# Optimization experiments

Hardware: AMD Instinct MI355X
Metric: run time of the kernel (lower is better)

The kernel has to match this reference:

```python
import jax, jax.numpy as jnp
import numpy as np

WIN = 5  # mask_window_size


def gather_windows(indices, image, win):
    """Gather win x win windows of pixel features centered at each query index.
    indices: [Q, 2] (y, x) int; image: [H, W, F].
    Returns keys [Q, win, win, F] (zeros at out-of-bounds) and pad mask [Q, win, win]."""
    H, W = image.shape[0], image.shape[1]
    offs = jnp.arange(win) - win // 2
    yy = (indices[:, 0, None] + offs)[:, :, None]
    xx = (indices[:, 1, None] + offs)[:, None, :]
    pad = (yy < 0) | (yy >= H) | (xx < 0) | (xx >= W)
    yc = jnp.clip(yy, 0, H - 1)
    xc = jnp.clip(xx, 0, W - 1)
    keys = image[yc, xc]
    keys = jnp.where(pad[..., None], jnp.zeros((), keys.dtype), keys)
    return keys, pad


def mlp(x, w1, b1, w2, b2):
    return jax.nn.relu(x @ w1 + b1) @ w2 + b2


def setup_inputs() -> dict:
    key = jax.random.key(0)
    ks = jax.random.split(key, 8)
    Q, Dq, F, Hd = 16384, 128, 128, 256
    H, W = 1024, 1024
    return {
        "queries": jax.random.normal(ks[0], (Q, Dq), jnp.float32),
        "query_indices": jax.random.randint(ks[1], (Q, 2), 0, H),
        "image": jax.random.normal(ks[2], (H, W, F), jnp.float32),
        "pm_w1": jax.random.normal(ks[3], (F, Hd), jnp.float32) * 0.02,
        "pm_b1": jnp.zeros((Hd,), jnp.float32),
        "pm_w2": jax.random.normal(ks[4], (Hd, Dq), jnp.float32) * 0.02,
        "pm_b2": jnp.zeros((Dq,), jnp.float32),
        "qp_w1": jax.random.normal(ks[5], (Dq, Hd), jnp.float32) * 0.02,
        "qp_b1": jnp.zeros((Hd,), jnp.float32),
        "qp_w2": jax.random.normal(ks[6], (Hd, F), jnp.float32) * 0.02,
        "qp_b2": jnp.zeros((F,), jnp.float32),
    }


def reference(queries, query_indices, image, pm_w1, pm_b1, pm_w2, pm_b2,
              qp_w1, qp_b1, qp_w2, qp_b2):
    # windowed key gather with out-of-bounds padding
    mask_keys, key_pad_mask = gather_windows(query_indices, image, WIN)  # [Q,w,w,F]
    # pixel_mask_head on gathered keys: F -> hidden -> query_dim
    mlped_mask_keys = mlp(mask_keys, pm_w1, pm_b1, pm_w2, pm_b2)          # [Q,w,w,Dq]
    binary_mask_logits = jnp.einsum('qf,qhwf->qhw', queries, mlped_mask_keys)
    # query_portion_head on queries: query_dim -> hidden -> F
    mlped_queries = mlp(queries, qp_w1, qp_b1, qp_w2, qp_b2)              # [Q,F]
    portion_logits = jnp.einsum('qf,qhwf->qhw', mlped_queries, mask_keys)
    # additive -inf pad bias (matches masked_fill + add in torch)
    pad_bias = jnp.where(key_pad_mask, -jnp.inf, 0.0).astype(binary_mask_logits.dtype)
    binary_mask_logits = binary_mask_logits + pad_bias
    portion_logits = portion_logits + pad_bias
    nonzero_key_mask = jnp.any(mask_keys != 0, axis=-1)
    return binary_mask_logits, portion_logits, nonzero_key_mask
```

## Files before the change

### kernel.cpp

```cpp
#include <hip/hip_runtime.h>
#include <math.h>

#define NEG_SENTINEL (-3.0e38f)


typedef __bf16 bf16_t;
typedef __bf16 bf16x8 __attribute__((ext_vector_type(8)));
typedef float  f32x4  __attribute__((ext_vector_type(4)));

#define MFMA(a, b, c) __builtin_amdgcn_mfma_f32_16x16x32_bf16((a), (b), (c), 0, 0, 0)

__device__ inline bf16x8 cvt_bf16x8(float4 a, float4 b) {
  bf16x8 r;
  r[0] = (bf16_t)a.x; r[1] = (bf16_t)a.y; r[2] = (bf16_t)a.z; r[3] = (bf16_t)a.w;
  r[4] = (bf16_t)b.x; r[5] = (bf16_t)b.y; r[6] = (bf16_t)b.z; r[7] = (bf16_t)b.w;
  return r;
}

__global__ __launch_bounds__(256) void prep_kernel(
    const float* __restrict__ pm_w1, const float* __restrict__ qp_w1,
    const float* __restrict__ qp_w2, const float* __restrict__ pm_w2,
    bf16_t* __restrict__ w1t, bf16_t* __restrict__ qw1t,
    bf16_t* __restrict__ qw2t, bf16_t* __restrict__ w2pm)
{
  int i = blockIdx.x * 256 + threadIdx.x;
  int m = i >> 15, e = i & 32767;
  if (m == 0)      { int n = e >> 7, k = e & 127; w1t[e]  = (bf16_t)pm_w1[k * 256 + n]; }
  else if (m == 1) { int n = e >> 7, k = e & 127; qw1t[e] = (bf16_t)qp_w1[k * 256 + n]; }
  else if (m == 2) { int f = e >> 8, h = e & 255; qw2t[e] = (bf16_t)qp_w2[h * 128 + f]; }
  else             { w2pm[e] = (bf16_t)pm_w2[e]; }
}

__global__ __launch_bounds__(256) void query_side_kernel(
    const float* __restrict__ queries,
    const float* __restrict__ pm_b2,
    const float* __restrict__ qp_b1, const float* __restrict__ qp_b2,
    const bf16_t* __restrict__ qw1t, const bf16_t* __restrict__ w2pm,
    const bf16_t* __restrict__ qw2t,
    bf16_t* __restrict__ v_ws, bf16_t* __restrict__ mq_ws, float* __restrict__ c_ws)
{
  __shared__ float qb1_lds[256];
  __shared__ float qb2_lds[128];
  __shared__ __align__(16) bf16_t hq_lds[4][4096];

  const int t = threadIdx.x;
  const int w = t >> 6, l = t & 63, lr = l & 15, lg = l >> 4;
  const int qb = blockIdx.x * 64;
  const int qrow = qb + w * 16 + lr;

  for (int i = t; i < 256; i += 256) qb1_lds[i] = qp_b1[i];
  if (t < 128) qb2_lds[t] = qp_b2[t];

  bf16x8 aq[4];
  float cpart = 0.f;
  const float* qp = queries + (size_t)qrow * 128;
  #pragma unroll
  for (int s = 0; s < 4; ++s) {
    int k0 = s * 32 + lg * 8;
    float4 u0 = *(const float4*)(qp + k0);
    float4 u1 = *(const float4*)(qp + k0 + 4);
    float4 b0 = *(const float4*)(pm_b2 + k0);
    float4 b1 = *(const float4*)(pm_b2 + k0 + 4);
    cpart += u0.x*b0.x + u0.y*b0.y + u0.z*b0.z + u0.w*b0.w
           + u1.x*b1.x + u1.y*b1.y + u1.z*b1.z + u1.w*b1.w;
    aq[s] = cvt_bf16x8(u0, u1);
  }
  cpart += __shfl_xor(cpart, 16);
  cpart += __shfl_xor(cpart, 32);
  if (l < 16) c_ws[qb + w * 16 + l] = cpart;

  __syncthreads();

  bf16_t* hqw = hq_lds[w];

  #pragma unroll 2
  for (int n = 0; n < 16; ++n) {
    f32x4 aa = {0.f, 0.f, 0.f, 0.f};
    f32x4 ac = {0.f, 0.f, 0.f, 0.f};
    const int col = n * 16 + lr;
    #pragma unroll
    for (int s = 0; s < 4; ++s) {
      bf16x8 ba = *(const bf16x8*)(qw1t + (size_t)col * 128 + (s * 4 + lg) * 8);
      bf16x8 bc = *(const bf16x8*)(w2pm + (size_t)col * 128 + (s * 4 + lg) * 8);
      aa = MFMA(aq[s], ba, aa);
      ac = MFMA(aq[s], bc, ac);
    }
    float bv = qb1_lds[col];
    const int k8 = col >> 3;
    #pragma unroll
    for (int j = 0; j < 4; ++j) {
      int rw = lg * 4 + j;
      float hv = fmaxf(aa[j] + bv, 0.f);
      hqw[rw * 256 + ((k8 ^ rw) * 8) + (col & 7)] = (bf16_t)hv;
      v_ws[(size_t)(qb + w * 16 + rw) * 256 + col] = (bf16_t)ac[j];
    }
  }

  __syncthreads();

  bf16x8 ah[8];
  #pragma unroll
  for (int s = 0; s < 8; ++s)
    ah[s] = *(const bf16x8*)(hqw + lr * 256 + (((s * 4 + lg) ^ lr) * 8));
  #pragma unroll 2
  for (int n = 0; n < 8; ++n) {
    f32x4 am = {0.f, 0.f, 0.f, 0.f};
    const int col = n * 16 + lr;
    #pragma unroll
    for (int s = 0; s < 8; ++s) {
      bf16x8 bm = *(const bf16x8*)(qw2t + (size_t)col * 256 + (s * 4 + lg) * 8);
      am = MFMA(ah[s], bm, am);
    }
    float bv = qb2_lds[col];
    #pragma unroll
    for (int j = 0; j < 4; ++j)
      mq_ws[(size_t)(qb + w * 16 + lg * 4 + j) * 128 + col] = (bf16_t)(am[j] + bv);
  }
}

__global__ __launch_bounds__(320, 2) void window_kernel(
    const int* __restrict__ qidx, const float* __restrict__ image,
    const float* __restrict__ pm_b1,
    const bf16_t* __restrict__ w1t_g,
    const bf16_t* __restrict__ v_ws, const bf16_t* __restrict__ mq_ws,
    const float* __restrict__ c_ws, float* __restrict__ out, int Q)
{
  __shared__ __align__(16) float v_lds[16 * 256];
  __shared__ __align__(16) float mq_lds[16 * 128];
  __shared__ float b1_lds[256];
  __shared__ float c_lds[16];
  __shared__ unsigned char pad_lds[400];

  const int t = threadIdx.x;
  const int w = t >> 6, l = t & 63, lr = l & 15, lg = l >> 4;
  const int qb = blockIdx.x * 16;

  bf16x8 afr[5][4];
  int aq[5], apad[5], nzf[5];
  #pragma unroll
  for (int tt = 0; tt < 5; ++tt) {
    int r = w * 80 + tt * 16 + lr;
    int ql = r / 25;
    int cell = r - ql * 25;
    int dy = cell / 5 - 2;
    int dx = cell - (dy + 2) * 5 - 2;
    int yy = qidx[2 * (qb + ql) + 0] + dy;
    int xx = qidx[2 * (qb + ql) + 1] + dx;
    bool pad = (yy < 0) | (yy >= 1024) | (xx < 0) | (xx >= 1024);
    aq[tt] = ql; apad[tt] = pad ? 1 : 0;
    if (l < 16) pad_lds[r] = (unsigned char)(pad ? 1 : 0);
    const float* px = image + (size_t)(pad ? 0 : (yy * 1024 + xx)) * 128;
    int nz = 0;
    #pragma unroll
    for (int s = 0; s < 4; ++s) {
      float4 u0 = make_float4(0.f, 0.f, 0.f, 0.f), u1 = u0;
      if (!pad) {
        u0 = *(const float4*)(px + s * 32 + lg * 8);
        u1 = *(const float4*)(px + s * 32 + lg * 8 + 4);
      }
      nz |= (u0.x != 0.f) | (u0.y != 0.f) | (u0.z != 0.f) | (u0.w != 0.f)
          | (u1.x != 0.f) | (u1.y != 0.f) | (u1.z != 0.f) | (u1.w != 0.f);
      afr[tt][s] = cvt_bf16x8(u0, u1);
    }
    nzf[tt] = nz;
  }

  {
    const bf16_t* vg = v_ws + (size_t)qb * 256;
    for (int i = t; i < 512; i += 320) {
      bf16x8 d = *(const bf16x8*)(vg + i * 8);
      float4 lo = make_float4((float)d[0], (float)d[1], (float)d[2], (float)d[3]);
      float4 hi = make_float4((float)d[4], (float)d[5], (float)d[6], (float)d[7]);
      *(float4*)(v_lds + i * 8) = lo;
      *(float4*)(v_lds + i * 8 + 4) = hi;
    }
  }
  {
    const bf16_t* mg = mq_ws + (size_t)qb * 128;
    for (int i = t; i < 256; i += 320) {
      bf16x8 d = *(const bf16x8*)(mg + i * 8);
      float4 lo = make_float4((float)d[0], (float)d[1], (float)d[2], (float)d[3]);
      float4 hi = make_float4((float)d[4], (float)d[5], (float)d[6], (float)d[7]);
      *(float4*)(mq_lds + i * 8) = lo;
      *(float4*)(mq_lds + i * 8 + 4) = hi;
    }
  }
  for (int i = t; i < 256; i += 320) b1_lds[i] = pm_b1[i];
  if (t < 16) c_lds[t] = c_ws[qb + t];

  __syncthreads();

  #pragma unroll
  for (int tt = 0; tt < 5; ++tt) {
    const float* mrow = mq_lds + aq[tt] * 128;
    float pp = 0.f;
    #pragma unroll
    for (int s = 0; s < 4; ++s) {
      const float* m = mrow + s * 32 + lg * 8;
      float4 m0 = *(const float4*)(m);
      float4 m1 = *(const float4*)(m + 4);
      bf16x8 a = afr[tt][s];
      pp += (float)a[0]*m0.x + (float)a[1]*m0.y + (float)a[2]*m0.z + (float)a[3]*m0.w
          + (float)a[4]*m1.x + (float)a[5]*m1.y + (float)a[6]*m1.z + (float)a[7]*m1.w;
    }
    pp += __shfl_xor(pp, 16);
    pp += __shfl_xor(pp, 32);
    int nz = nzf[tt];
    nz |= __shfl_xor(nz, 16);
    nz |= __shfl_xor(nz, 32);
    if (l < 16) {
      int r = w * 80 + tt * 16 + l;
      int ql = aq[tt];
      int cell = r - ql * 25;
      int q = qb + ql;
      out[(size_t)Q * 25 + (size_t)q * 25 + cell]     = apad[tt] ? NEG_SENTINEL : pp;
      out[(size_t)2 * Q * 25 + (size_t)q * 25 + cell] = nz ? 1.0f : 0.0f;
    }
  }

  int vb[5][4];
  #pragma unroll
  for (int tt = 0; tt < 5; ++tt) {
    #pragma unroll
    for (int j = 0; j < 4; ++j) {
      int rc = w * 80 + tt * 16 + lg * 4 + j;
      vb[tt][j] = (rc / 25) * 256 + lr;
    }
  }
  float part[5][4];
  #pragma unroll
  for (int tt = 0; tt < 5; ++tt)
    #pragma unroll
    for (int j = 0; j < 4; ++j) part[tt][j] = 0.f;

  #pragma unroll 2
  for (int n = 0; n < 16; ++n) {
    bf16x8 b[4];
    #pragma unroll
    for (int s = 0; s < 4; ++s)
      b[s] = *(const bf16x8*)(w1t_g + (size_t)(n * 16 + lr) * 128 + (s * 4 + lg) * 8);
    float bv = b1_lds[n * 16 + lr];
    #pragma unroll
    for (int tt = 0; tt < 5; ++tt) {
      f32x4 acc = {0.f, 0.f, 0.f, 0.f};
      #pragma unroll
      for (int s = 0; s < 4; ++s) acc = MFMA(afr[tt][s], b[s], acc);
      #pragma unroll
      for (int j = 0; j < 4; ++j) {
        float hv = fmaxf(acc[j] + bv, 0.f);
        part[tt][j] = fmaf(hv, v_lds[vb[tt][j] + n * 16], part[tt][j]);
      }
    }
  }

  #pragma unroll
  for (int tt = 0; tt < 5; ++tt) {
    #pragma unroll
    for (int j = 0; j < 4; ++j) {
      float s = part[tt][j];
      s += __shfl_xor(s, 1);
      s += __shfl_xor(s, 2);
      s += __shfl_xor(s, 4);
      s += __shfl_xor(s, 8);
      if (lr == 0) {
        int rc = w * 80 + tt * 16 + lg * 4 + j;
        int q = rc / 25, cell = rc - q * 25;
        out[(size_t)(qb + q) * 25 + cell] =
            pad_lds[rc] ? NEG_SENTINEL : (s + c_lds[q]);
      }
    }
  }
}

extern "C" void kernel_launch(void* const* d_in, const int* in_sizes, int n_in,
                              void* d_out, int out_size, void* d_ws, size_t ws_size,
                              hipStream_t stream) {
  const float* queries = (const float*)d_in[0];
  const int*   qidx    = (const int*)d_in[1];
  const float* image   = (const float*)d_in[2];
  const float* pm_w1   = (const float*)d_in[3];
  const float* pm_b1   = (const float*)d_in[4];
  const float* pm_w2   = (const float*)d_in[5];
  const float* pm_b2   = (const float*)d_in[6];
  const float* qp_w1   = (const float*)d_in[7];
  const float* qp_b1   = (const float*)d_in[8];
  const float* qp_w2   = (const float*)d_in[9];
  const float* qp_b2   = (const float*)d_in[10];
  float* out = (float*)d_out;

  const int Q = in_sizes[0] / 128;

  char* ws = (char*)d_ws;
  bf16_t* v_ws  = (bf16_t*)ws;  ws += (size_t)Q * 256 * 2;
  bf16_t* mq_ws = (bf16_t*)ws;  ws += (size_t)Q * 128 * 2;
  float*  c_ws  = (float*)ws;   ws += (size_t)Q * 4;
  bf16_t* w1t   = (bf16_t*)ws;  ws += 32768 * 2;
  bf16_t* qw1t  = (bf16_t*)ws;  ws += 32768 * 2;
  bf16_t* qw2t  = (bf16_t*)ws;  ws += 32768 * 2;
  bf16_t* w2pm  = (bf16_t*)ws;  ws += 32768 * 2;

  prep_kernel<<<512, 256, 0, stream>>>(pm_w1, qp_w1, qp_w2, pm_w2,
                                       w1t, qw1t, qw2t, w2pm);
  query_side_kernel<<<Q / 64, 256, 0, stream>>>(queries, pm_b2, qp_b1, qp_b2,
                                                qw1t, w2pm, qw2t, v_ws, mq_ws, c_ws);
  window_kernel<<<Q / 16, 320, 0, stream>>>(qidx, image, pm_b1, w1t,
                                            v_ws, mq_ws, c_ws, out, Q);
}
```

Measured before the change: 733.6 us.

## Fuse query-side MLP into window kernel, computing per-block query results in LDS

Drops the separate query-side kernel. Each 16-query window block now computes its own query MLP, the W2-projected query vector and the bias dot product with four of its five waves, and keeps the results in LDS instead of a global workspace. This removes a kernel launch and the bf16 round trip of the v/mq/c intermediates through global memory. In exchange it adds LDS usage (an extra hq buffer, bias arrays) and two more block barriers, and the query-side MFMA work now runs at 16 queries per block with the fifth wave idle during it.

New measurement: 729.2 us. About the same (-0.6%).

```diff
diff --git a/kernel.cpp b/kernel.cpp
--- a/kernel.cpp
+++ b/kernel.cpp
@@ -31,102 +31,20 @@
   else             { w2pm[e] = (bf16_t)pm_w2[e]; }
 }
 
-__global__ __launch_bounds__(256) void query_side_kernel(
+__global__ __launch_bounds__(320, 2) void fused_kernel(
     const float* __restrict__ queries,
-    const float* __restrict__ pm_b2,
+    const int* __restrict__ qidx, const float* __restrict__ image,
+    const float* __restrict__ pm_b1, const float* __restrict__ pm_b2,
     const float* __restrict__ qp_b1, const float* __restrict__ qp_b2,
-    const bf16_t* __restrict__ qw1t, const bf16_t* __restrict__ w2pm,
-    const bf16_t* __restrict__ qw2t,
-    bf16_t* __restrict__ v_ws, bf16_t* __restrict__ mq_ws, float* __restrict__ c_ws)
-{
-  __shared__ float qb1_lds[256];
-  __shared__ float qb2_lds[128];
-  __shared__ __align__(16) bf16_t hq_lds[4][4096];
-
-  const int t = threadIdx.x;
-  const int w = t >> 6, l = t & 63, lr = l & 15, lg = l >> 4;
-  const int qb = blockIdx.x * 64;
-  const int qrow = qb + w * 16 + lr;
-
-  for (int i = t; i < 256; i += 256) qb1_lds[i] = qp_b1[i];
-  if (t < 128) qb2_lds[t] = qp_b2[t];
-
-  bf16x8 aq[4];
-  float cpart = 0.f;
-  const float* qp = queries + (size_t)qrow * 128;
-  #pragma unroll
-  for (int s = 0; s < 4; ++s) {
-    int k0 = s * 32 + lg * 8;
-    float4 u0 = *(const float4*)(qp + k0);
-    float4 u1 = *(const float4*)(qp + k0 + 4);
-    float4 b0 = *(const float4*)(pm_b2 + k0);
-    float4 b1 = *(const float4*)(pm_b2 + k0 + 4);
-    cpart += u0.x*b0.x + u0.y*b0.y + u0.z*b0.z + u0.w*b0.w
-           + u1.x*b1.x + u1.y*b1.y + u1.z*b1.z + u1.w*b1.w;
-    aq[s] = cvt_bf16x8(u0, u1);
-  }
-  cpart += __shfl_xor(cpart, 16);
-  cpart += __shfl_xor(cpart, 32);
-  if (l < 16) c_ws[qb + w * 16 + l] = cpart;
-
-  __syncthreads();
-
-  bf16_t* hqw = hq_lds[w];
-
-  #pragma unroll 2
-  for (int n = 0; n < 16; ++n) {
-    f32x4 aa = {0.f, 0.f, 0.f, 0.f};
-    f32x4 ac = {0.f, 0.f, 0.f, 0.f};
-    const int col = n * 16 + lr;
-    #pragma unroll
-    for (int s = 0; s < 4; ++s) {
-      bf16x8 ba = *(const bf16x8*)(qw1t + (size_t)col * 128 + (s * 4 + lg) * 8);
-      bf16x8 bc = *(const bf16x8*)(w2pm + (size_t)col * 128 + (s * 4 + lg) * 8);
-      aa = MFMA(aq[s], ba, aa);
-      ac = MFMA(aq[s], bc, ac);
-    }
-    float bv = qb1_lds[col];
-    const int k8 = col >> 3;
-    #pragma unroll
-    for (int j = 0; j < 4; ++j) {
-      int rw = lg * 4 + j;
-      float hv = fmaxf(aa[j] + bv, 0.f);
-      hqw[rw * 256 + ((k8 ^ rw) * 8) + (col & 7)] = (bf16_t)hv;
-      v_ws[(size_t)(qb + w * 16 + rw) * 256 + col] = (bf16_t)ac[j];
-    }
-  }
-
-  __syncthreads();
-
-  bf16x8 ah[8];
-  #pragma unroll
-  for (int s = 0; s < 8; ++s)
-    ah[s] = *(const bf16x8*)(hqw + lr * 256 + (((s * 4 + lg) ^ lr) * 8));
-  #pragma unroll 2
-  for (int n = 0; n < 8; ++n) {
-    f32x4 am = {0.f, 0.f, 0.f, 0.f};
-    const int col = n * 16 + lr;
-    #pragma unroll
-    for (int s = 0; s < 8; ++s) {
-      bf16x8 bm = *(const bf16x8*)(qw2t + (size_t)col * 256 + (s * 4 + lg) * 8);
-      am = MFMA(ah[s], bm, am);
-    }
-    float bv = qb2_lds[col];
-    #pragma unroll
-    for (int j = 0; j < 4; ++j)
-      mq_ws[(size_t)(qb + w * 16 + lg * 4 + j) * 128 + col] = (bf16_t)(am[j] + bv);
-  }
-}
-
-__global__ __launch_bounds__(320, 2) void window_kernel(
-    const int* __restrict__ qidx, const float* __restrict__ image,
-    const float* __restrict__ pm_b1,
-    const bf16_t* __restrict__ w1t_g,
-    const bf16_t* __restrict__ v_ws, const bf16_t* __restrict__ mq_ws,
-    const float* __restrict__ c_ws, float* __restrict__ out, int Q)
+    const bf16_t* __restrict__ w1t_g, const bf16_t* __restrict__ qw1t,
+    const bf16_t* __restrict__ w2pm, const bf16_t* __restrict__ qw2t,
+    float* __restrict__ out, int Q)
 {
   __shared__ __align__(16) float v_lds[16 * 256];
   __shared__ __align__(16) float mq_lds[16 * 128];
+  __shared__ __align__(16) bf16_t hq_lds[16 * 256];
+  __shared__ float qb1_lds[256];
+  __shared__ float qb2_lds[128];
   __shared__ float b1_lds[256];
   __shared__ float c_lds[16];
   __shared__ unsigned char pad_lds[400];
@@ -135,8 +53,11 @@
   const int w = t >> 6, l = t & 63, lr = l & 15, lg = l >> 4;
   const int qb = blockIdx.x * 16;
 
+  for (int i = t; i < 256; i += 320) { qb1_lds[i] = qp_b1[i]; b1_lds[i] = pm_b1[i]; }
+  if (t < 128) qb2_lds[t] = qp_b2[t];
+
   bf16x8 afr[5][4];
-  int aq[5], apad[5], nzf[5];
+  int aqv[5], apad[5], nzf[5];
   #pragma unroll
   for (int tt = 0; tt < 5; ++tt) {
     int r = w * 80 + tt * 16 + lr;
@@ -147,7 +68,7 @@
     int yy = qidx[2 * (qb + ql) + 0] + dy;
     int xx = qidx[2 * (qb + ql) + 1] + dx;
     bool pad = (yy < 0) | (yy >= 1024) | (xx < 0) | (xx >= 1024);
-    aq[tt] = ql; apad[tt] = pad ? 1 : 0;
+    aqv[tt] = ql; apad[tt] = pad ? 1 : 0;
     if (l < 16) pad_lds[r] = (unsigned char)(pad ? 1 : 0);
     const float* px = image + (size_t)(pad ? 0 : (yy * 1024 + xx)) * 128;
     int nz = 0;
@@ -165,34 +86,81 @@
     nzf[tt] = nz;
   }
 
-  {
-    const bf16_t* vg = v_ws + (size_t)qb * 256;
-    for (int i = t; i < 512; i += 320) {
-      bf16x8 d = *(const bf16x8*)(vg + i * 8);
-      float4 lo = make_float4((float)d[0], (float)d[1], (float)d[2], (float)d[3]);
-      float4 hi = make_float4((float)d[4], (float)d[5], (float)d[6], (float)d[7]);
-      *(float4*)(v_lds + i * 8) = lo;
-      *(float4*)(v_lds + i * 8 + 4) = hi;
-    }
-  }
-  {
-    const bf16_t* mg = mq_ws + (size_t)qb * 128;
-    for (int i = t; i < 256; i += 320) {
-      bf16x8 d = *(const bf16x8*)(mg + i * 8);
-      float4 lo = make_float4((float)d[0], (float)d[1], (float)d[2], (float)d[3]);
-      float4 hi = make_float4((float)d[4], (float)d[5], (float)d[6], (float)d[7]);
-      *(float4*)(mq_lds + i * 8) = lo;
-      *(float4*)(mq_lds + i * 8 + 4) = hi;
-    }
-  }
-  for (int i = t; i < 256; i += 320) b1_lds[i] = pm_b1[i];
-  if (t < 16) c_lds[t] = c_ws[qb + t];
+  bf16x8 aq[4];
+  if (w < 4) {
+    float cpart = 0.f;
+    const float* qp = queries + (size_t)(qb + lr) * 128;
+    #pragma unroll
+    for (int s = 0; s < 4; ++s) {
+      int k0 = s * 32 + lg * 8;
+      float4 u0 = *(const float4*)(qp + k0);
+      float4 u1 = *(const float4*)(qp + k0 + 4);
+      float4 b0 = *(const float4*)(pm_b2 + k0);
+      float4 b1 = *(const float4*)(pm_b2 + k0 + 4);
+      cpart += u0.x*b0.x + u0.y*b0.y + u0.z*b0.z + u0.w*b0.w
+             + u1.x*b1.x + u1.y*b1.y + u1.z*b1.z + u1.w*b1.w;
+      aq[s] = cvt_bf16x8(u0, u1);
+    }
+    cpart += __shfl_xor(cpart, 16);
+    cpart += __shfl_xor(cpart, 32);
+    if (w == 0 && l < 16) c_lds[l] = cpart;
+  }
 
   __syncthreads();
 
-  #pragma unroll
-  for (int tt = 0; tt < 5; ++tt) {
-    const float* mrow = mq_lds + aq[tt] * 128;
+  if (w < 4) {
+    #pragma unroll
+    for (int n = 0; n < 4; ++n) {
+      f32x4 aa = {0.f, 0.f, 0.f, 0.f};
+      f32x4 ac = {0.f, 0.f, 0.f, 0.f};
+      const int col = w * 64 + n * 16 + lr;
+      #pragma unroll
+      for (int s = 0; s < 4; ++s) {
+        bf16x8 ba = *(const bf16x8*)(qw1t + (size_t)col * 128 + (s * 4 + lg) * 8);
+        bf16x8 bc = *(const bf16x8*)(w2pm + (size_t)col * 128 + (s * 4 + lg) * 8);
+        aa = MFMA(aq[s], ba, aa);
+        ac = MFMA(aq[s], bc, ac);
+      }
+      float bv = qb1_lds[col];
+      const int k8 = col >> 3;
+      #pragma unroll
+      for (int j = 0; j < 4; ++j) {
+        int rw = lg * 4 + j;
+        float hv = fmaxf(aa[j] + bv, 0.f);
+        hq_lds[rw * 256 + ((k8 ^ rw) * 8) + (col & 7)] = (bf16_t)hv;
+        v_lds[rw * 256 + col] = ac[j];
+      }
+    }
+  }
+
+  __syncthreads();
+
+  if (w < 4) {
+    bf16x8 ah[8];
+    #pragma unroll
+    for (int s = 0; s < 8; ++s)
+      ah[s] = *(const bf16x8*)(hq_lds + lr * 256 + (((s * 4 + lg) ^ lr) * 8));
+    #pragma unroll
+    for (int n = 0; n < 2; ++n) {
+      f32x4 am = {0.f, 0.f, 0.f, 0.f};
+      const int col = w * 32 + n * 16 + lr;
+      #pragma unroll
+      for (int s = 0; s < 8; ++s) {
+        bf16x8 bm = *(const bf16x8*)(qw2t + (size_t)col * 256 + (s * 4 + lg) * 8);
+        am = MFMA(ah[s], bm, am);
+      }
+      float bv = qb2_lds[col];
+      #pragma unroll
+      for (int j = 0; j < 4; ++j)
+        mq_lds[(lg * 4 + j) * 128 + col] = am[j] + bv;
+    }
+  }
+
+  __syncthreads();
+
+  #pragma unroll
+  for (int tt = 0; tt < 5; ++tt) {
+    const float* mrow = mq_lds + aqv[tt] * 128;
     float pp = 0.f;
     #pragma unroll
     for (int s = 0; s < 4; ++s) {
@@ -205,16 +173,16 @@
     }
     pp += __shfl_xor(pp, 16);
     pp += __shfl_xor(pp, 32);
-    int nz = nzf[tt];
-    nz |= __shfl_xor(nz, 16);
-    nz |= __shfl_xor(nz, 32);
+    int nzr = nzf[tt];
+    nzr |= __shfl_xor(nzr, 16);
+    nzr |= __shfl_xor(nzr, 32);
     if (l < 16) {
       int r = w * 80 + tt * 16 + l;
-      int ql = aq[tt];
+      int ql = aqv[tt];
       int cell = r - ql * 25;
       int q = qb + ql;
       out[(size_t)Q * 25 + (size_t)q * 25 + cell]     = apad[tt] ? NEG_SENTINEL : pp;
-      out[(size_t)2 * Q * 25 + (size_t)q * 25 + cell] = nz ? 1.0f : 0.0f;
+      out[(size_t)2 * Q * 25 + (size_t)q * 25 + cell] = nzr ? 1.0f : 0.0f;
     }
   }
 
@@ -291,9 +259,6 @@
   const int Q = in_sizes[0] / 128;
 
   char* ws = (char*)d_ws;
-  bf16_t* v_ws  = (bf16_t*)ws;  ws += (size_t)Q * 256 * 2;
-  bf16_t* mq_ws = (bf16_t*)ws;  ws += (size_t)Q * 128 * 2;
-  float*  c_ws  = (float*)ws;   ws += (size_t)Q * 4;
   bf16_t* w1t   = (bf16_t*)ws;  ws += 32768 * 2;
   bf16_t* qw1t  = (bf16_t*)ws;  ws += 32768 * 2;
   bf16_t* qw2t  = (bf16_t*)ws;  ws += 32768 * 2;
@@ -301,8 +266,7 @@
 
   prep_kernel<<<512, 256, 0, stream>>>(pm_w1, qp_w1, qp_w2, pm_w2,
                                        w1t, qw1t, qw2t, w2pm);
-  query_side_kernel<<<Q / 64, 256, 0, stream>>>(queries, pm_b2, qp_b1, qp_b2,
-                                                qw1t, w2pm, qw2t, v_ws, mq_ws, c_ws);
-  window_kernel<<<Q / 16, 320, 0, stream>>>(qidx, image, pm_b1, w1t,
-                                            v_ws, mq_ws, c_ws, out, Q);
-}
+  fused_kernel<<<Q / 16, 320, 0, stream>>>(queries, qidx, image,
+                                           pm_b1, pm_b2, qp_b1, qp_b2,
+                                           w1t, qw1t, w2pm, qw2t, out, Q);
+}
```
